# Kernel optimization log

Measured on AMD Instinct MI355X. Metric: run time of the kernel, lower is better.

## Reference

```python
import jax, jax.numpy as jnp
import numpy as np
import math

B, S, D, H = 2, 2048, 2048, 16
HD = D // H  # 128


def _rope(x, cos, sin):
    # x: [b, s, h, hd]; cos/sin: [s, hd//2]
    # torch view_as_complex pairs adjacent elements: (even=real, odd=imag)
    xr = x[..., 0::2]
    xi = x[..., 1::2]
    c = cos[None, :, None, :]
    s = sin[None, :, None, :]
    out_r = xr * c - xi * s
    out_i = xr * s + xi * c
    # interleave back: [..., hd//2, 2] -> [..., hd]
    return jnp.stack([out_r, out_i], axis=-1).reshape(x.shape)


def setup_inputs() -> dict:
    key = jax.random.key(0)
    ks = jax.random.split(key, 5)
    x = jax.random.normal(ks[0], (B, S, D), dtype=jnp.float32)
    std = 1.0 / math.sqrt(D)
    wq = jax.random.normal(ks[1], (D, D), dtype=jnp.float32) * std
    wk = jax.random.normal(ks[2], (D, D), dtype=jnp.float32) * std
    wv = jax.random.normal(ks[3], (D, D), dtype=jnp.float32) * std
    wo = jax.random.normal(ks[4], (D, D), dtype=jnp.float32) * std
    # RoPE frequencies, theta = 10000
    freqs = 1.0 / (10000.0 ** (jnp.arange(0, HD, 2, dtype=jnp.float32) / HD))  # [hd//2]
    t = jnp.arange(S, dtype=jnp.float32)
    angles = jnp.outer(t, freqs)  # [s, hd//2]
    freqs_cos = jnp.cos(angles)
    freqs_sin = jnp.sin(angles)
    # causal additive mask [s, s]
    mask = jnp.triu(jnp.full((S, S), -jnp.inf, dtype=jnp.float32), k=1)
    return {"x": x, "start_pos": 0, "freqs_cos": freqs_cos, "freqs_sin": freqs_sin,
            "mask": mask, "wq": wq, "wk": wk, "wv": wv, "wo": wo}


def reference(x, start_pos, freqs_cos, freqs_sin, mask, wq, wk, wv, wo):
    b, s, d = x.shape
    # projections (torch Linear: y = x @ W.T)
    xq = (x @ wq.T).reshape(b, s, H, HD)
    xk = (x @ wk.T).reshape(b, s, H, HD)
    xv = (x @ wv.T).reshape(b, s, H, HD)
    xq = _rope(xq, freqs_cos, freqs_sin)
    xk = _rope(xk, freqs_cos, freqs_sin)
    # start_pos = 0 prefill: cache[:b, :s] == freshly computed xk/xv
    # scores: [b, h, s_q, s_k]
    scores = jnp.einsum("bqhd,bkhd->bhqk", xq, xk) / math.sqrt(HD)
    scores = scores + mask[None, None, :, :]
    probs = jax.nn.softmax(scores, axis=-1)
    out = jnp.einsum("bhqk,bkhd->bqhd", probs, xv).reshape(b, s, d)
    return out @ wo.T
```

## Files before the change

### kernel.cpp

```cpp
#include <hip/hip_runtime.h>

typedef __attribute__((ext_vector_type(8))) short short8;
typedef __attribute__((ext_vector_type(4))) float f32x4;
typedef __attribute__((ext_vector_type(16))) float f32x16;
typedef unsigned int u32;
typedef __attribute__((ext_vector_type(4))) u32 u32x4;
typedef unsigned short u16;

#define DEV __device__ __forceinline__

DEV void async16(const void* g, void* l) {
  __builtin_amdgcn_global_load_lds((const __attribute__((address_space(1))) u32*)g,
                                   (__attribute__((address_space(3))) u32*)l, 16, 0, 0);
}

DEV u16 f2bf(float f) {
  u32 u = __builtin_bit_cast(u32, f);
  u32 r = (u + 0x7FFFu + ((u >> 16) & 1u)) >> 16;
  return (u16)r;
}
DEV float bf2f(u16 h) { return __builtin_bit_cast(float, (u32)h << 16); }

DEV u32 cvtpk(float lo, float hi) {
  u32 r;
  asm("v_cvt_pk_bf16_f32 %0, %1, %2" : "=v"(r) : "v"(lo), "v"(hi));
  return r;
}

#define RAW_BARRIER() asm volatile("s_barrier" ::: "memory")
#define VMWAIT(N) asm volatile("s_waitcnt vmcnt(" #N ")" ::: "memory")

__global__ void cast_all_kernel(const float* __restrict__ x, const float* __restrict__ wq,
                                const float* __restrict__ wk, const float* __restrict__ wv,
                                const float* __restrict__ wo, u16* __restrict__ out) {
  constexpr int XN = 2097152;
  constexpr int WN = 1048576;
  constexpr int TOT = XN + 4 * WN;
  int stride = gridDim.x * blockDim.x;
  for (int i = blockIdx.x * blockDim.x + threadIdx.x; i < TOT; i += stride) {
    const float* src;
    int off;
    if (i < XN) {
      src = x; off = i;
    } else {
      int j = i - XN, wsel = j >> 20;
      const float* ws4[4] = {wq, wk, wv, wo};
      src = ws4[wsel]; off = j & (WN - 1);
    }
    float4 v = reinterpret_cast<const float4*>(src)[off];
    ushort4 o = make_ushort4(f2bf(v.x), f2bf(v.y), f2bf(v.z), f2bf(v.w));
    reinterpret_cast<ushort4*>(out)[i] = o;
  }
}

__global__ __launch_bounds__(512, 2) void gemm_qkv8(const u16* __restrict__ A,
                                                    const u16* __restrict__ Bw,
                                                    u16* __restrict__ q_ws,
                                                    u16* __restrict__ k_ws,
                                                    u16* __restrict__ vt_ws,
                                                    const float* __restrict__ cbp,
                                                    const float* __restrict__ sbp) {
  constexpr int K = 2048, NT = 32;
  __shared__ char sm[131072];
  const int tid = threadIdx.x, lane = tid & 63, w = tid >> 6;
  const int wm = w >> 2, wn = w & 3;
  const int bid = blockIdx.x;
  const int n = (bid & 7) * 48 + (bid >> 3);
  const int row0 = (n & 15) * 256, col0 = (n >> 4) * 256;

  f32x4 acc[2][2][4][2] = {};

  auto stage_chunk = [&](int bufoff, int chunk, int k0) {
    const bool isA = (chunk == 0) || (chunk == 3);
    const u16* src = isA ? A : Bw;
    const int h = isA ? ((chunk == 3) ? 1 : 0) : (chunk - 1);
    const int rbase = (isA ? row0 : col0) + h * 128;
    const int ldsbase = bufoff + (isA ? 0 : 32768) + h * 16384;
#pragma unroll
    for (int i = 0; i < 2; ++i) {
      int slot = tid + i * 512;
      int r = slot >> 3, cs = slot & 7;
      async16(src + (size_t)(rbase + r) * K + k0 + ((cs ^ (r & 7)) << 3),
              sm + ldsbase + slot * 16);
    }
  };

  short8 af[4][2], bf0[2][2], bf1[2][2];
  auto ldA = [&](int base, int ha) {
#pragma unroll
    for (int mi = 0; mi < 4; ++mi) {
      int row = ha * 128 + wm * 64 + mi * 16 + (lane & 15);
#pragma unroll
      for (int kk = 0; kk < 2; ++kk)
        af[mi][kk] = *reinterpret_cast<const short8*>(
            sm + base + row * 128 + ((((kk << 2) + (lane >> 4)) ^ (row & 7)) << 4));
    }
  };
  auto ldB = [&](short8 (&bf)[2][2], int base, int hb) {
#pragma unroll
    for (int ni = 0; ni < 2; ++ni) {
      int row = hb * 128 + wn * 32 + ni * 16 + (lane & 15);
#pragma unroll
      for (int kk = 0; kk < 2; ++kk)
        bf[ni][kk] = *reinterpret_cast<const short8*>(
            sm + base + 32768 + row * 128 + ((((kk << 2) + (lane >> 4)) ^ (row & 7)) << 4));
    }
  };

#define MFMA16(HA, HB, BF)                                                              \
  __builtin_amdgcn_s_setprio(1);                                                        \
  _Pragma("unroll") for (int mi = 0; mi < 4; ++mi)                                      \
      _Pragma("unroll") for (int ni = 0; ni < 2; ++ni)                                  \
          _Pragma("unroll") for (int kk = 0; kk < 2; ++kk)                              \
              acc[HA][HB][mi][ni] = __builtin_amdgcn_mfma_f32_16x16x32_bf16(            \
                  af[mi][kk], BF[ni][kk], acc[HA][HB][mi][ni], 0, 0, 0);                \
  __builtin_amdgcn_s_setprio(0);

  stage_chunk(0, 0, 0);
  stage_chunk(0, 1, 0);
  stage_chunk(0, 2, 0);
  stage_chunk(0, 3, 0);
  VMWAIT(0);
  RAW_BARRIER();

  for (int t = 0; t < NT - 1; ++t) {
    const int cb_ = (t & 1) * 65536, nb = ((t + 1) & 1) * 65536;
    const int k0n = (t + 1) * 64;
    ldA(cb_, 0);
    ldB(bf0, cb_, 0);
    stage_chunk(nb, 0, k0n);
    RAW_BARRIER();
    MFMA16(0, 0, bf0);
    VMWAIT(4);
    RAW_BARRIER();
    ldB(bf1, cb_, 1);
    stage_chunk(nb, 1, k0n);
    RAW_BARRIER();
    MFMA16(0, 1, bf1);
    VMWAIT(4);
    RAW_BARRIER();
    ldA(cb_, 1);
    stage_chunk(nb, 2, k0n);
    RAW_BARRIER();
    MFMA16(1, 0, bf0);
    RAW_BARRIER();
    stage_chunk(nb, 3, k0n);
    RAW_BARRIER();
    MFMA16(1, 1, bf1);
    VMWAIT(4);
    RAW_BARRIER();
  }
  {
    const int cb_ = ((NT - 1) & 1) * 65536;
    ldA(cb_, 0);
    ldB(bf0, cb_, 0);
    RAW_BARRIER();
    MFMA16(0, 0, bf0);
    VMWAIT(0);
    RAW_BARRIER();
    ldB(bf1, cb_, 1);
    RAW_BARRIER();
    MFMA16(0, 1, bf1);
    RAW_BARRIER();
    ldA(cb_, 1);
    RAW_BARRIER();
    MFMA16(1, 0, bf0);
    RAW_BARRIER();
    MFMA16(1, 1, bf1);
  }

  const float rs = 0.127517436f;
#pragma unroll
  for (int ha = 0; ha < 2; ++ha)
#pragma unroll
    for (int hb = 0; hb < 2; ++hb)
#pragma unroll
      for (int mi = 0; mi < 4; ++mi)
#pragma unroll
        for (int ni = 0; ni < 2; ++ni)
#pragma unroll
          for (int rr = 0; rr < 4; ++rr) {
            int gm = row0 + ha * 128 + wm * 64 + mi * 16 + ((lane >> 4) << 2) + rr;
            int gn = col0 + hb * 128 + wn * 32 + ni * 16 + (lane & 15);
            float v = acc[ha][hb][mi][ni][rr];
            int tsel = gn >> 11, nn = gn & 2047;
            int b = gm >> 11, s = gm & 2047, h = nn >> 7, hd = nn & 127;
            if (tsel < 2) {
              float pv = __shfl_xor(v, 1, 64);
              float c = cbp[(s << 6) + (hd >> 1)];
              float sn = sbp[(s << 6) + (hd >> 1)];
              float o = (hd & 1) ? (pv * sn + v * c) : (v * c - pv * sn);
              if (tsel == 0) o *= rs;
              u16* dst = tsel ? k_ws : q_ws;
              dst[(size_t)((b << 4) | h) * 262144 + (s << 7) + hd] = f2bf(o);
            } else {
              vt_ws[(size_t)((b << 4) | h) * 262144 + (hd << 11) + s] = f2bf(v);
            }
          }
#undef MFMA16
}

__global__ __launch_bounds__(256) void gemm_bt(const u16* __restrict__ A,
                                               const u16* __restrict__ Bw,
                                               float* __restrict__ C) {
  constexpr int K = 2048;
  __shared__ char sm[32768];
  const int tid = threadIdx.x;
  const int lane = tid & 63;
  const int w = tid >> 6;
  const int by = blockIdx.x & 31;
  const int bx = blockIdx.x >> 5;
  const int row0 = by * 128, col0 = bx * 128;
  const int wr = (w >> 1) * 64, wc = (w & 1) * 64;
  f32x4 acc[4][4] = {};

  for (int k0 = 0; k0 < K; k0 += 64) {
    __syncthreads();
#pragma unroll
    for (int i = 0; i < 4; ++i) {
      int slot = tid + i * 256;
      int r = slot >> 3, s = slot & 7;
      int sl = s ^ (r & 7);
      async16(A + (size_t)(row0 + r) * K + (k0 + sl * 8), sm + slot * 16);
    }
#pragma unroll
    for (int i = 0; i < 4; ++i) {
      int slot = tid + i * 256;
      int r = slot >> 3, s = slot & 7;
      int sl = s ^ (r & 7);
      async16(Bw + (size_t)(col0 + r) * K + (k0 + sl * 8), sm + 16384 + slot * 16);
    }
    __syncthreads();
#pragma unroll
    for (int kk = 0; kk < 2; ++kk) {
      short8 af[4], bfr[4];
#pragma unroll
      for (int mi = 0; mi < 4; ++mi) {
        int r = wr + mi * 16 + (lane & 15);
        int ps = (kk * 4 + (lane >> 4)) ^ (r & 7);
        af[mi] = *reinterpret_cast<const short8*>(sm + r * 128 + ps * 16);
      }
#pragma unroll
      for (int ni = 0; ni < 4; ++ni) {
        int r = wc + ni * 16 + (lane & 15);
        int ps = (kk * 4 + (lane >> 4)) ^ (r & 7);
        bfr[ni] = *reinterpret_cast<const short8*>(sm + 16384 + r * 128 + ps * 16);
      }
#pragma unroll
      for (int mi = 0; mi < 4; ++mi)
#pragma unroll
        for (int ni = 0; ni < 4; ++ni)
          acc[mi][ni] = __builtin_amdgcn_mfma_f32_16x16x32_bf16(af[mi], bfr[ni], acc[mi][ni], 0, 0, 0);
    }
  }
#pragma unroll
  for (int mi = 0; mi < 4; ++mi)
#pragma unroll
    for (int ni = 0; ni < 4; ++ni)
#pragma unroll
      for (int r = 0; r < 4; ++r) {
        int gm = row0 + wr + mi * 16 + ((lane >> 4) << 2) + r;
        int gn = col0 + wc + ni * 16 + (lane & 15);
        C[((size_t)gm << 11) + gn] = acc[mi][ni][r];
      }
}

__global__ __launch_bounds__(256, 2) void attn_kernel(const u16* __restrict__ q_ws,
                                                      const u16* __restrict__ k_ws,
                                                      const u16* __restrict__ vt_ws,
                                                      u16* __restrict__ attn_ws) {
  constexpr int S = 2048;
  constexpr float NEGBIG = -3.0e38f;
  __shared__ char sm[65536];
  const int tid = threadIdx.x, lane = tid & 63, w = tid >> 6;
  const int hi = lane >> 5, l31 = lane & 31;
  const int bid = blockIdx.x;
  const int qtr = bid >> 5;
  const int qt = (qtr < 8) ? qtr : 23 - qtr;
  const int bh = ((bid & 7) << 2) | ((bid >> 3) & 3);
  const int qr0 = qt * 128 + w * 32;
  const int ntile = 2 * qt + 2;
  const int my_nt = (qr0 >> 6) + 1;

  const u16* qp = q_ws + (size_t)bh * S * 128;
  const u16* kp = k_ws + (size_t)bh * S * 128;
  const u16* vp = vt_ws + (size_t)bh * 128 * S;

  short8 qf[8];
  {
    const u16* qr = qp + (size_t)(qr0 + l31) * 128 + hi * 8;
#pragma unroll
    for (int ks = 0; ks < 8; ++ks) qf[ks] = *reinterpret_cast<const short8*>(qr + ks * 16);
  }
  f32x16 accO[4];
#pragma unroll
  for (int dc = 0; dc < 4; ++dc)
#pragma unroll
    for (int r = 0; r < 16; ++r) accO[dc][r] = 0.f;
  float m = -1e30f, l = 0.f;

  auto stage = [&](int bufoff, int kv0) {
#pragma unroll
    for (int i = 0; i < 4; ++i) {
      int slot = tid + i * 256;
      int r = slot >> 4, s = slot & 15;
      async16(kp + (size_t)(kv0 + r) * 128 + ((s ^ (r & 15)) * 8), sm + bufoff + slot * 16);
    }
#pragma unroll
    for (int i = 0; i < 4; ++i) {
      int slot = tid + i * 256;
      int r = slot >> 3, s = slot & 7;
      async16(vp + (size_t)r * S + kv0 + ((s ^ (r & 7)) * 8), sm + bufoff + 16384 + slot * 16);
    }
  };

  stage(0, 0);
  __syncthreads();

  for (int t = 0; t < ntile; ++t) {
    const char* kb = sm + (t & 1) * 32768;
    const char* vb = kb + 16384;
    if (t + 1 < ntile) stage(((t + 1) & 1) * 32768, (t + 1) * 64);

    if (t < my_nt) {
      f32x16 sacc[2];
#pragma unroll
      for (int jc = 0; jc < 2; ++jc)
#pragma unroll
        for (int r = 0; r < 16; ++r) sacc[jc][r] = 0.f;
      __builtin_amdgcn_s_setprio(1);
#pragma unroll
      for (int jc = 0; jc < 2; ++jc) {
        const char* krp = kb + (jc * 32 + l31) * 256;
        const int sw = l31 & 15;
#pragma unroll
        for (int ks = 0; ks < 8; ++ks) {
          short8 kf = *reinterpret_cast<const short8*>(krp + (((2 * ks + hi) ^ sw) << 4));
          sacc[jc] = __builtin_amdgcn_mfma_f32_32x32x16_bf16(kf, qf[ks], sacc[jc], 0, 0, 0);
        }
      }
      __builtin_amdgcn_s_setprio(0);
      if (t == my_nt - 1) {
#pragma unroll
        for (int jc = 0; jc < 2; ++jc) {
          int thr = qr0 + l31 - t * 64 - 32 * jc - 4 * hi;
#pragma unroll
          for (int r = 0; r < 16; ++r) {
            int c0 = (r & 3) + 8 * (r >> 2);
            if (c0 > thr) sacc[jc][r] = NEGBIG;
          }
        }
      }
      float pmA = NEGBIG, pmB = NEGBIG, pmC = NEGBIG, pmD = NEGBIG;
#pragma unroll
      for (int jc = 0; jc < 2; ++jc)
#pragma unroll
        for (int r = 0; r < 16; r += 4) {
          pmA = fmaxf(pmA, sacc[jc][r]);
          pmB = fmaxf(pmB, sacc[jc][r + 1]);
          pmC = fmaxf(pmC, sacc[jc][r + 2]);
          pmD = fmaxf(pmD, sacc[jc][r + 3]);
        }
      float pmax = fmaxf(fmaxf(pmA, pmB), fmaxf(pmC, pmD));
      pmax = fmaxf(pmax, __shfl_xor(pmax, 32, 64));
      if (!__all(pmax - m <= 8.0f)) {
        float mnew = fmaxf(m, pmax);
        float scl = exp2f(m - mnew);
        m = mnew;
        l *= scl;
#pragma unroll
        for (int dc = 0; dc < 4; ++dc)
#pragma unroll
          for (int r = 0; r < 16; ++r) accO[dc][r] *= scl;
      }
      float sA = 0.f, sB = 0.f, sC = 0.f, sD = 0.f;
#pragma unroll
      for (int jc = 0; jc < 2; ++jc)
#pragma unroll
        for (int r = 0; r < 16; r += 4) {
          float p0 = exp2f(sacc[jc][r] - m);
          float p1 = exp2f(sacc[jc][r + 1] - m);
          float p2 = exp2f(sacc[jc][r + 2] - m);
          float p3 = exp2f(sacc[jc][r + 3] - m);
          sacc[jc][r] = p0; sacc[jc][r + 1] = p1; sacc[jc][r + 2] = p2; sacc[jc][r + 3] = p3;
          sA += p0; sB += p1; sC += p2; sD += p3;
        }
      float ps = (sA + sB) + (sC + sD);
      ps += __shfl_xor(ps, 32, 64);
      l += ps;
      short8 pfrag[4];
#pragma unroll
      for (int ks = 0; ks < 4; ++ks) {
        const int jc = ks >> 1, u8 = (ks & 1) * 8;
        u32 wA = cvtpk(sacc[jc][u8 + 0], sacc[jc][u8 + 1]);
        u32 wB = cvtpk(sacc[jc][u8 + 2], sacc[jc][u8 + 3]);
        u32 wC = cvtpk(sacc[jc][u8 + 4], sacc[jc][u8 + 5]);
        u32 wD = cvtpk(sacc[jc][u8 + 6], sacc[jc][u8 + 7]);
        u32 qA = __shfl_xor(wA, 32, 64);
        u32 qB = __shfl_xor(wB, 32, 64);
        u32 qC = __shfl_xor(wC, 32, 64);
        u32 qD = __shfl_xor(wD, 32, 64);
        u32x4 t4;
        t4.x = hi ? qC : wA;
        t4.y = hi ? qD : wB;
        t4.z = hi ? wC : qA;
        t4.w = hi ? wD : qB;
        pfrag[ks] = __builtin_bit_cast(short8, t4);
      }
      __builtin_amdgcn_s_setprio(1);
#pragma unroll
      for (int ks = 0; ks < 4; ++ks) {
#pragma unroll
        for (int dc = 0; dc < 4; ++dc) {
          const char* vrp = vb + (dc * 32 + l31) * 128;
          short8 vf = *reinterpret_cast<const short8*>(vrp + (((2 * ks + hi) ^ (l31 & 7)) << 4));
          accO[dc] = __builtin_amdgcn_mfma_f32_32x32x16_bf16(vf, pfrag[ks], accO[dc], 0, 0, 0);
        }
      }
      __builtin_amdgcn_s_setprio(0);
    }
    __syncthreads();
  }

  const int b = bh >> 4, h = bh & 15;
  char* tb = sm + w * 8192;
  float inv = (l > 0.f) ? 1.0f / l : 0.f;
#pragma unroll
  for (int dc = 0; dc < 4; ++dc)
#pragma unroll
    for (int r = 0; r < 16; ++r) {
      int d = dc * 32 + (r & 3) + 8 * (r >> 2) + 4 * hi;
      int byte = l31 * 256 + d * 2;
      *reinterpret_cast<u16*>(tb + (byte ^ ((l31 & 7) << 4))) = f2bf(accO[dc][r] * inv);
    }
  asm volatile("s_waitcnt lgkmcnt(0)" ::: "memory");
#pragma unroll
  for (int i = 0; i < 8; ++i) {
    int r = i * 4 + (lane >> 4);
    int s = lane & 15;
    f32x4 v = *reinterpret_cast<const f32x4*>(tb + r * 256 + ((s ^ (r & 7)) << 4));
    size_t addr = ((size_t)(b * 2048 + qr0 + r) << 11) + (h << 7) + s * 8;
    *reinterpret_cast<f32x4*>(attn_ws + addr) = v;
  }
}

extern "C" void kernel_launch(void* const* d_in, const int* in_sizes, int n_in,
                              void* d_out, int out_size, void* d_ws, size_t ws_size,
                              hipStream_t stream) {
  const float* x = (const float*)d_in[0];
  const float* cb = (const float*)d_in[2];
  const float* sb = (const float*)d_in[3];
  const float* wq = (const float*)d_in[5];
  const float* wk = (const float*)d_in[6];
  const float* wv = (const float*)d_in[7];
  const float* wo = (const float*)d_in[8];

  char* p = (char*)d_ws;
  u16* xb  = (u16*)p; p += (size_t)4096 * 2048 * 2;
  u16* wqb = (u16*)p; p += (size_t)2048 * 2048 * 2;
  u16* wkb = (u16*)p; p += (size_t)2048 * 2048 * 2;
  u16* wvb = (u16*)p; p += (size_t)2048 * 2048 * 2;
  u16* wob = (u16*)p; p += (size_t)2048 * 2048 * 2;
  u16* q_ws = (u16*)p; p += (size_t)4096 * 2048 * 2;
  u16* k_ws = (u16*)p; p += (size_t)4096 * 2048 * 2;
  u16* vt_ws = (u16*)p; p += (size_t)4096 * 2048 * 2;
  u16* attn_ws = xb;
  (void)wkb; (void)wvb;

  cast_all_kernel<<<3072, 256, 0, stream>>>(x, wq, wk, wv, wo, xb);

  gemm_qkv8<<<384, 512, 0, stream>>>(xb, wqb, q_ws, k_ws, vt_ws, cb, sb);

  attn_kernel<<<512, 256, 0, stream>>>(q_ws, k_ws, vt_ws, attn_ws);

  gemm_bt<<<512, 256, 0, stream>>>(attn_ws, wob, (float*)d_out);
}
```

Baseline: 296.7 us.

## Deepen QKV GEMM LDS pipeline with per-quarter-tile staging and XCD-aware tile mapping

Restructures the QKV projection GEMM main loop so each 64-wide K slice is staged in four independent quarter-tile chunks whose loads are issued further ahead. Fewer barriers are needed per iteration and more global loads stay in flight while MFMAs run. The loop is unrolled by two K-steps with explicit vmcnt waits. It also changes the block-to-tile mapping so each XCD works on a contiguous 8x6 patch of output tiles, which should improve L2 reuse of A and B rows. The cost is a more intricate wait-count schedule that is easy to get wrong and can cause data races.

```diff
diff --git a/kernel.cpp b/kernel.cpp
--- a/kernel.cpp
+++ b/kernel.cpp
@@ -60,50 +60,47 @@
                                                     u16* __restrict__ vt_ws,
                                                     const float* __restrict__ cbp,
                                                     const float* __restrict__ sbp) {
-  constexpr int K = 2048, NT = 32;
+  constexpr int K = 2048, NITER = 16;
   __shared__ char sm[131072];
   const int tid = threadIdx.x, lane = tid & 63, w = tid >> 6;
   const int wm = w >> 2, wn = w & 3;
   const int bid = blockIdx.x;
-  const int n = (bid & 7) * 48 + (bid >> 3);
-  const int row0 = (n & 15) * 256, col0 = (n >> 4) * 256;
+  const int xcd = bid & 7, jj = bid >> 3;
+  const int mt = (xcd & 1) * 8 + (jj & 7);
+  const int ntc = (xcd >> 1) * 6 + (jj >> 3);
+  const int row0 = mt * 256, col0 = ntc * 256;
 
   f32x4 acc[2][2][4][2] = {};
 
-  auto stage_chunk = [&](int bufoff, int chunk, int k0) {
-    const bool isA = (chunk == 0) || (chunk == 3);
-    const u16* src = isA ? A : Bw;
-    const int h = isA ? ((chunk == 3) ? 1 : 0) : (chunk - 1);
-    const int rbase = (isA ? row0 : col0) + h * 128;
-    const int ldsbase = bufoff + (isA ? 0 : 32768) + h * 16384;
+  auto stage = [&](int slotbase, const u16* src, int rbase, int k0) {
 #pragma unroll
     for (int i = 0; i < 2; ++i) {
       int slot = tid + i * 512;
       int r = slot >> 3, cs = slot & 7;
       async16(src + (size_t)(rbase + r) * K + k0 + ((cs ^ (r & 7)) << 3),
-              sm + ldsbase + slot * 16);
+              sm + slotbase + slot * 16);
     }
   };
 
   short8 af[4][2], bf0[2][2], bf1[2][2];
-  auto ldA = [&](int base, int ha) {
+  auto ldA = [&](int slotbase) {
 #pragma unroll
     for (int mi = 0; mi < 4; ++mi) {
-      int row = ha * 128 + wm * 64 + mi * 16 + (lane & 15);
+      int row = wm * 64 + mi * 16 + (lane & 15);
 #pragma unroll
       for (int kk = 0; kk < 2; ++kk)
         af[mi][kk] = *reinterpret_cast<const short8*>(
-            sm + base + row * 128 + ((((kk << 2) + (lane >> 4)) ^ (row & 7)) << 4));
+            sm + slotbase + row * 128 + ((((kk << 2) + (lane >> 4)) ^ (row & 7)) << 4));
     }
   };
-  auto ldB = [&](short8 (&bf)[2][2], int base, int hb) {
+  auto ldB = [&](short8 (&bf)[2][2], int slotbase) {
 #pragma unroll
     for (int ni = 0; ni < 2; ++ni) {
-      int row = hb * 128 + wn * 32 + ni * 16 + (lane & 15);
+      int row = wn * 32 + ni * 16 + (lane & 15);
 #pragma unroll
       for (int kk = 0; kk < 2; ++kk)
         bf[ni][kk] = *reinterpret_cast<const short8*>(
-            sm + base + 32768 + row * 128 + ((((kk << 2) + (lane >> 4)) ^ (row & 7)) << 4));
+            sm + slotbase + row * 128 + ((((kk << 2) + (lane >> 4)) ^ (row & 7)) << 4));
     }
   };
 
@@ -116,56 +113,67 @@
                   af[mi][kk], BF[ni][kk], acc[HA][HB][mi][ni], 0, 0, 0);                \
   __builtin_amdgcn_s_setprio(0);
 
-  stage_chunk(0, 0, 0);
-  stage_chunk(0, 1, 0);
-  stage_chunk(0, 2, 0);
-  stage_chunk(0, 3, 0);
-  VMWAIT(0);
-  RAW_BARRIER();
-
-  for (int t = 0; t < NT - 1; ++t) {
-    const int cb_ = (t & 1) * 65536, nb = ((t + 1) & 1) * 65536;
-    const int k0n = (t + 1) * 64;
-    ldA(cb_, 0);
-    ldB(bf0, cb_, 0);
-    stage_chunk(nb, 0, k0n);
-    RAW_BARRIER();
+  stage(0, A, row0, 0);
+  stage(32768, Bw, col0, 0);
+  stage(49152, Bw, col0 + 128, 0);
+  stage(16384, A, row0 + 128, 0);
+  stage(65536, A, row0, 64);
+  stage(65536 + 32768, Bw, col0, 64);
+
+  for (int i = 0; i < NITER - 1; ++i) {
+    const int kT1 = i * 128 + 64, kN = (i + 1) * 128;
+    VMWAIT(8); RAW_BARRIER();
+    ldA(0); ldB(bf0, 32768);
+    stage(65536 + 49152, Bw, col0 + 128, kT1);
     MFMA16(0, 0, bf0);
-    VMWAIT(4);
-    RAW_BARRIER();
-    ldB(bf1, cb_, 1);
-    stage_chunk(nb, 1, k0n);
-    RAW_BARRIER();
+    VMWAIT(8); RAW_BARRIER();
+    ldB(bf1, 49152);
+    stage(65536 + 16384, A, row0 + 128, kT1);
     MFMA16(0, 1, bf1);
-    VMWAIT(4);
-    RAW_BARRIER();
-    ldA(cb_, 1);
-    stage_chunk(nb, 2, k0n);
-    RAW_BARRIER();
+    VMWAIT(8); RAW_BARRIER();
+    ldA(16384);
+    stage(0, A, row0, kN);
+    stage(32768, Bw, col0, kN);
     MFMA16(1, 0, bf0);
-    RAW_BARRIER();
-    stage_chunk(nb, 3, k0n);
-    RAW_BARRIER();
     MFMA16(1, 1, bf1);
-    VMWAIT(4);
-    RAW_BARRIER();
+    VMWAIT(8); RAW_BARRIER();
+    ldA(65536); ldB(bf0, 65536 + 32768);
+    stage(49152, Bw, col0 + 128, kN);
+    MFMA16(0, 0, bf0);
+    VMWAIT(8); RAW_BARRIER();
+    ldB(bf1, 65536 + 49152);
+    stage(16384, A, row0 + 128, kN);
+    MFMA16(0, 1, bf1);
+    VMWAIT(8); RAW_BARRIER();
+    ldA(65536 + 16384);
+    stage(65536, A, row0, kN + 64);
+    stage(65536 + 32768, Bw, col0, kN + 64);
+    MFMA16(1, 0, bf0);
+    MFMA16(1, 1, bf1);
   }
   {
-    const int cb_ = ((NT - 1) & 1) * 65536;
-    ldA(cb_, 0);
-    ldB(bf0, cb_, 0);
-    RAW_BARRIER();
+    const int kT1 = (NITER - 1) * 128 + 64;
+    VMWAIT(8); RAW_BARRIER();
+    ldA(0); ldB(bf0, 32768);
+    stage(65536 + 49152, Bw, col0 + 128, kT1);
     MFMA16(0, 0, bf0);
-    VMWAIT(0);
-    RAW_BARRIER();
-    ldB(bf1, cb_, 1);
-    RAW_BARRIER();
+    VMWAIT(8); RAW_BARRIER();
+    ldB(bf1, 49152);
+    stage(65536 + 16384, A, row0 + 128, kT1);
     MFMA16(0, 1, bf1);
-    RAW_BARRIER();
-    ldA(cb_, 1);
-    RAW_BARRIER();
+    VMWAIT(8); RAW_BARRIER();
+    ldA(16384);
     MFMA16(1, 0, bf0);
-    RAW_BARRIER();
+    MFMA16(1, 1, bf1);
+    VMWAIT(4); RAW_BARRIER();
+    ldA(65536); ldB(bf0, 65536 + 32768);
+    MFMA16(0, 0, bf0);
+    VMWAIT(2); RAW_BARRIER();
+    ldB(bf1, 65536 + 49152);
+    MFMA16(0, 1, bf1);
+    VMWAIT(0); RAW_BARRIER();
+    ldA(65536 + 16384);
+    MFMA16(1, 0, bf0);
     MFMA16(1, 1, bf1);
   }
 
```

New measurement: 293.9 us. About the same (-1.0%).
